# Optimization experiments

Hardware: AMD Instinct MI355X
Metric: run time of the kernel (lower is better)

Reference implementation:

```python
import jax, jax.numpy as jnp
import numpy as np

B = 4096
D_IN = 2048
D_H = 2048
W_SCALE = 0.02  # keep exp() gate pre-activations small / numerically safe


def setup_inputs() -> dict:
    key = jax.random.key(0)
    ks = jax.random.split(key, 16)
    inp = {
        "x": jax.random.normal(ks[0], (B, D_IN), jnp.float32),
        "h_prev": jax.random.normal(ks[1], (B, D_H), jnp.float32),
        "c_prev": jax.random.normal(ks[2], (B, D_H), jnp.float32),
        "n_prev": jax.random.uniform(ks[3], (B, D_H), jnp.float32),
    }
    # input->hidden weights (stored [in, out]; torch Linear computes x @ W.T + b,
    # equivalent to x @ W_here + b) and biases
    for i, name in enumerate(["i", "f", "o", "z"]):
        inp[f"W_{name}"] = jax.random.normal(ks[4 + i], (D_IN, D_H), jnp.float32) * W_SCALE
        inp[f"b_{name}"] = jax.random.normal(ks[8 + i], (D_H,), jnp.float32) * W_SCALE
        inp[f"U_{name}"] = jax.random.normal(ks[12 + i], (D_H, D_H), jnp.float32) * W_SCALE
    return inp


def reference(x, h_prev, c_prev, n_prev,
              W_i, b_i, U_i, W_f, b_f, U_f,
              W_o, b_o, U_o, W_z, b_z, U_z):
    # Gate pre-activations: 8 GEMMs fused pairwise per gate
    i = jnp.exp(x @ W_i + b_i + h_prev @ U_i)
    f = jnp.exp(x @ W_f + b_f + h_prev @ U_f)
    o = jax.nn.sigmoid(x @ W_o + b_o + h_prev @ U_o)
    z = jnp.tanh(x @ W_z + b_z + h_prev @ U_z)
    c = f * c_prev + i * z
    n = f * n_prev + i
    h = o * (c / (n + 1e-6))
    return (h, c, n)
```

## Files before the change

kernel.cpp:

```cpp
#include <hip/hip_runtime.h>
#include <hip/hip_bf16.h>
#include <stdint.h>

#define B_DIM 4096
#define DH    2048
#define K_DIM 4096
#define N_DIM 8192

typedef __bf16  bf16x8 __attribute__((ext_vector_type(8)));
typedef float   f32x4  __attribute__((ext_vector_type(4)));

__device__ __forceinline__ unsigned short f2bf(float f) {
  unsigned int u = __float_as_uint(f);
  u += 0x7FFFu + ((u >> 16) & 1u);
  return (unsigned short)(u >> 16);
}

__global__ void cast_cat_A(const float* __restrict__ x, const float* __restrict__ h,
                           unsigned short* __restrict__ Abuf) {
  int idx = blockIdx.x * 256 + threadIdx.x;
  const int half = B_DIM * (DH / 4);
  bool isx = (idx < half);
  int i2 = isx ? idx : idx - half;
  int b  = i2 >> 9;
  int c4 = i2 & 511;
  const float* src = (isx ? x : h) + (((size_t)b) << 11) + (c4 << 2);
  float4 v = *(const float4*)src;
  ushort4 o;
  o.x = f2bf(v.x); o.y = f2bf(v.y); o.z = f2bf(v.z); o.w = f2bf(v.w);
  int col = (isx ? 0 : DH) + (c4 << 2);
  *(ushort4*)(Abuf + (size_t)b * K_DIM + col) = o;
}

__global__ void transpose_cast_B(const float* __restrict__ Wi, const float* __restrict__ Ui,
                                 const float* __restrict__ Wf, const float* __restrict__ Uf,
                                 const float* __restrict__ Wo, const float* __restrict__ Uo,
                                 const float* __restrict__ Wz, const float* __restrict__ Uz,
                                 unsigned short* __restrict__ Bt) {
  __shared__ unsigned short lds[64 * 68];
  const int k0 = blockIdx.x * 64;
  const int n0 = blockIdx.y * 64;
  const int g  = n0 >> 11;
  const int j0 = n0 & 2047;
  const float* W = (g == 0) ? Wi : (g == 1) ? Wf : (g == 2) ? Wo : Wz;
  const float* U = (g == 0) ? Ui : (g == 1) ? Uf : (g == 2) ? Uo : Uz;
  const float* src = ((k0 < DH) ? (W + (size_t)k0 * DH)
                                : (U + (size_t)(k0 - DH) * DH)) + j0;
  const int t = threadIdx.x;
  #pragma unroll
  for (int r = 0; r < 4; ++r) {
    int slot = r * 256 + t;
    int kk = slot >> 4;
    int c4 = slot & 15;
    float4 v = *(const float4*)(src + (size_t)kk * DH + (c4 << 2));
    int n = c4 << 2;
    lds[(n + 0) * 68 + kk] = f2bf(v.x);
    lds[(n + 1) * 68 + kk] = f2bf(v.y);
    lds[(n + 2) * 68 + kk] = f2bf(v.z);
    lds[(n + 3) * 68 + kk] = f2bf(v.w);
  }
  __syncthreads();
  #pragma unroll
  for (int r = 0; r < 4; ++r) {
    int slot = r * 256 + t;
    int nn = slot >> 4;
    int c8 = slot & 15;
    *(ushort4*)(Bt + (size_t)(n0 + nn) * K_DIM + k0 + (c8 << 2)) =
        *(const ushort4*)(lds + nn * 68 + (c8 << 2));
  }
}

__global__ __launch_bounds__(256, 3) void gemm_bt(const unsigned short* __restrict__ A,
                                                  const unsigned short* __restrict__ Bt,
                                                  float* __restrict__ C) {
  __shared__ alignas(16) unsigned short As[128 * 32];
  __shared__ alignas(16) unsigned short Bs[128 * 32];
  const int t    = threadIdx.x;
  const int wave = t >> 6;
  const int lane = t & 63;
  const int m0 = blockIdx.y * 128;
  const int n0 = blockIdx.x * 128;
  const int wm = (wave & 1) * 64;
  const int wn = (wave >> 1) * 64;
  const int lm = lane & 15;
  const int kg = lane >> 4;

  f32x4 acc[4][4] = {};

  const int c0 = t, c1 = t + 256;
  const unsigned short* pa0 = A  + (size_t)(m0 + (c0 >> 2)) * K_DIM + (c0 & 3) * 8;
  const unsigned short* pa1 = A  + (size_t)(m0 + (c1 >> 2)) * K_DIM + (c1 & 3) * 8;
  const unsigned short* pb0 = Bt + (size_t)(n0 + (c0 >> 2)) * K_DIM + (c0 & 3) * 8;
  const unsigned short* pb1 = Bt + (size_t)(n0 + (c1 >> 2)) * K_DIM + (c1 & 3) * 8;
  unsigned short* lA0 = As + (wave * 64) * 8;
  unsigned short* lA1 = As + (256 + wave * 64) * 8;
  unsigned short* lB0 = Bs + (wave * 64) * 8;
  unsigned short* lB1 = Bs + (256 + wave * 64) * 8;

  const int aoff = (wm + lm) * 32 + kg * 8;
  const int boff = (wn + lm) * 32 + kg * 8;

  for (int k0 = 0; k0 < K_DIM; k0 += 32) {
    __builtin_amdgcn_global_load_lds((const __attribute__((address_space(1))) unsigned int*)(pa0 + k0),
                                     (__attribute__((address_space(3))) unsigned int*)lA0, 16, 0, 0);
    __builtin_amdgcn_global_load_lds((const __attribute__((address_space(1))) unsigned int*)(pa1 + k0),
                                     (__attribute__((address_space(3))) unsigned int*)lA1, 16, 0, 0);
    __builtin_amdgcn_global_load_lds((const __attribute__((address_space(1))) unsigned int*)(pb0 + k0),
                                     (__attribute__((address_space(3))) unsigned int*)lB0, 16, 0, 0);
    __builtin_amdgcn_global_load_lds((const __attribute__((address_space(1))) unsigned int*)(pb1 + k0),
                                     (__attribute__((address_space(3))) unsigned int*)lB1, 16, 0, 0);
    __syncthreads();
    bf16x8 av[4], bv[4];
    #pragma unroll
    for (int mi = 0; mi < 4; ++mi)
      av[mi] = *(const bf16x8*)(As + aoff + mi * 16 * 32);
    #pragma unroll
    for (int ni = 0; ni < 4; ++ni)
      bv[ni] = *(const bf16x8*)(Bs + boff + ni * 16 * 32);
    #pragma unroll
    for (int mi = 0; mi < 4; ++mi) {
      #pragma unroll
      for (int ni = 0; ni < 4; ++ni)
        acc[mi][ni] = __builtin_amdgcn_mfma_f32_16x16x32_bf16(av[mi], bv[ni], acc[mi][ni], 0, 0, 0);
    }
    __syncthreads();
  }

  #pragma unroll
  for (int mi = 0; mi < 4; ++mi) {
    #pragma unroll
    for (int ni = 0; ni < 4; ++ni) {
      float* p = C + (size_t)(m0 + wm + mi * 16 + kg * 4) * N_DIM + (n0 + wn + ni * 16 + lm);
      #pragma unroll
      for (int r = 0; r < 4; ++r)
        p[(size_t)r * N_DIM] = acc[mi][ni][r];
    }
  }
}

__global__ void gate_epilogue(const float* __restrict__ C,
                              const float* __restrict__ bi, const float* __restrict__ bfv,
                              const float* __restrict__ bo, const float* __restrict__ bz,
                              const float* __restrict__ cprev, const float* __restrict__ nprev,
                              float* __restrict__ out) {
  int idx = blockIdx.x * 256 + threadIdx.x;
  int b = idx >> 9;
  int j = (idx & 511) << 2;
  const float* base = C + (size_t)b * N_DIM + j;
  float4 pi = *(const float4*)(base);
  float4 pf = *(const float4*)(base + DH);
  float4 po = *(const float4*)(base + 2 * DH);
  float4 pz = *(const float4*)(base + 3 * DH);
  float4 vbi = *(const float4*)(bi + j);
  float4 vbf = *(const float4*)(bfv + j);
  float4 vbo = *(const float4*)(bo + j);
  float4 vbz = *(const float4*)(bz + j);
  size_t pidx = (((size_t)b) << 11) + j;
  float4 cp = *(const float4*)(cprev + pidx);
  float4 np = *(const float4*)(nprev + pidx);

  const float* Pi = (const float*)&pi; const float* Pf = (const float*)&pf;
  const float* Po = (const float*)&po; const float* Pz = (const float*)&pz;
  const float* Bi = (const float*)&vbi; const float* Bf = (const float*)&vbf;
  const float* Bo = (const float*)&vbo; const float* Bz = (const float*)&vbz;
  const float* Cp = (const float*)&cp; const float* Np = (const float*)&np;

  float rh[4], rc[4], rn[4];
  #pragma unroll
  for (int e = 0; e < 4; ++e) {
    float iv = __expf(Pi[e] + Bi[e]);
    float fv = __expf(Pf[e] + Bf[e]);
    float ao = Po[e] + Bo[e];
    float ov = 1.0f / (1.0f + __expf(-ao));
    float t2 = __expf(2.0f * (Pz[e] + Bz[e]));
    float zv = 1.0f - 2.0f / (t2 + 1.0f);
    float cv = fv * Cp[e] + iv * zv;
    float nv = fv * Np[e] + iv;
    rc[e] = cv; rn[e] = nv;
    rh[e] = ov * (cv / (nv + 1e-6f));
  }
  *(float4*)(out + pidx)            = make_float4(rh[0], rh[1], rh[2], rh[3]);
  *(float4*)(out + 8388608 + pidx)  = make_float4(rc[0], rc[1], rc[2], rc[3]);
  *(float4*)(out + 16777216 + pidx) = make_float4(rn[0], rn[1], rn[2], rn[3]);
}

extern "C" void kernel_launch(void* const* d_in, const int* in_sizes, int n_in,
                              void* d_out, int out_size, void* d_ws, size_t ws_size,
                              hipStream_t stream) {
  const float* x      = (const float*)d_in[0];
  const float* h_prev = (const float*)d_in[1];
  const float* c_prev = (const float*)d_in[2];
  const float* n_prev = (const float*)d_in[3];
  const float* W_i = (const float*)d_in[4];  const float* b_i = (const float*)d_in[5];  const float* U_i = (const float*)d_in[6];
  const float* W_f = (const float*)d_in[7];  const float* b_f = (const float*)d_in[8];  const float* U_f = (const float*)d_in[9];
  const float* W_o = (const float*)d_in[10]; const float* b_o = (const float*)d_in[11]; const float* U_o = (const float*)d_in[12];
  const float* W_z = (const float*)d_in[13]; const float* b_z = (const float*)d_in[14]; const float* U_z = (const float*)d_in[15];
  float* out = (float*)d_out;

  char* ws = (char*)d_ws;
  unsigned short* Abuf = (unsigned short*)ws;
  unsigned short* Bt   = (unsigned short*)(ws + 33554432);
  float*          Cpre = (float*)(ws + 33554432 + 67108864);

  cast_cat_A<<<16384, 256, 0, stream>>>(x, h_prev, Abuf);
  transpose_cast_B<<<dim3(64, 128), 256, 0, stream>>>(W_i, U_i, W_f, U_f, W_o, U_o, W_z, U_z, Bt);
  gemm_bt<<<dim3(64, 32), 256, 0, stream>>>(Abuf, Bt, Cpre);
  gate_epilogue<<<8192, 256, 0, stream>>>(Cpre, b_i, b_f, b_o, b_z, c_prev, n_prev, out);
}
```

Baseline: 649.9 us.

## Interleave gate columns in Bt and fuse gate epilogue into GEMM

Reorders the transposed weight rows so that each wave's four 16-column MFMA tiles hold the i, f, o, z gates for the same hidden units. The gate nonlinearities and state updates can then run directly on the GEMM accumulators. This removes the 128MB fp32 pre-activation buffer write and reread, along with the separate epilogue launch. In exchange, the epilogue now does scalar, strided global loads and stores per lane instead of float4 accesses, and adds register pressure to the GEMM kernel.

```diff
diff --git a/kernel.cpp b/kernel.cpp
--- a/kernel.cpp
+++ b/kernel.cpp
@@ -39,9 +39,8 @@
                                  unsigned short* __restrict__ Bt) {
   __shared__ unsigned short lds[64 * 68];
   const int k0 = blockIdx.x * 64;
-  const int n0 = blockIdx.y * 64;
-  const int g  = n0 >> 11;
-  const int j0 = n0 & 2047;
+  const int g  = blockIdx.y >> 5;
+  const int j0 = (blockIdx.y & 31) * 64;
   const float* W = (g == 0) ? Wi : (g == 1) ? Wf : (g == 2) ? Wo : Wz;
   const float* U = (g == 0) ? Ui : (g == 1) ? Uf : (g == 2) ? Uo : Uz;
   const float* src = ((k0 < DH) ? (W + (size_t)k0 * DH)
@@ -65,14 +64,19 @@
     int slot = r * 256 + t;
     int nn = slot >> 4;
     int c8 = slot & 15;
-    *(ushort4*)(Bt + (size_t)(n0 + nn) * K_DIM + k0 + (c8 << 2)) =
+    int j  = j0 + nn;
+    int np = ((j >> 5) << 7) + ((j & 16) << 2) + (g << 4) + (j & 15);
+    *(ushort4*)(Bt + (size_t)np * K_DIM + k0 + (c8 << 2)) =
         *(const ushort4*)(lds + nn * 68 + (c8 << 2));
   }
 }
 
-__global__ __launch_bounds__(256, 3) void gemm_bt(const unsigned short* __restrict__ A,
-                                                  const unsigned short* __restrict__ Bt,
-                                                  float* __restrict__ C) {
+__global__ __launch_bounds__(256, 3) void gemm_gates(const unsigned short* __restrict__ A,
+                                                     const unsigned short* __restrict__ Bt,
+                                                     const float* __restrict__ bi, const float* __restrict__ bf,
+                                                     const float* __restrict__ bo, const float* __restrict__ bz,
+                                                     const float* __restrict__ cprev, const float* __restrict__ nprev,
+                                                     float* __restrict__ out) {
   __shared__ alignas(16) unsigned short As[128 * 32];
   __shared__ alignas(16) unsigned short Bs[128 * 32];
   const int t    = threadIdx.x;
@@ -126,62 +130,30 @@
     __syncthreads();
   }
 
+  const int jj = (blockIdx.x << 5) + ((wn >> 6) << 4) + lm;
+  const float vbi = bi[jj], vbf = bf[jj], vbo = bo[jj], vbz = bz[jj];
   #pragma unroll
   for (int mi = 0; mi < 4; ++mi) {
+    const int mrow = m0 + wm + mi * 16 + kg * 4;
     #pragma unroll
-    for (int ni = 0; ni < 4; ++ni) {
-      float* p = C + (size_t)(m0 + wm + mi * 16 + kg * 4) * N_DIM + (n0 + wn + ni * 16 + lm);
-      #pragma unroll
-      for (int r = 0; r < 4; ++r)
-        p[(size_t)r * N_DIM] = acc[mi][ni][r];
+    for (int r = 0; r < 4; ++r) {
+      const size_t idx = (size_t)(mrow + r) * DH + jj;
+      float pi = acc[mi][0][r] + vbi;
+      float pf = acc[mi][1][r] + vbf;
+      float po = acc[mi][2][r] + vbo;
+      float pz = acc[mi][3][r] + vbz;
+      float iv = __expf(pi);
+      float fv = __expf(pf);
+      float ov = 1.0f / (1.0f + __expf(-po));
+      float t2 = __expf(2.0f * pz);
+      float zv = 1.0f - 2.0f / (t2 + 1.0f);
+      float cv = fv * cprev[idx] + iv * zv;
+      float nv = fv * nprev[idx] + iv;
+      out[idx]            = ov * (cv / (nv + 1e-6f));
+      out[8388608 + idx]  = cv;
+      out[16777216 + idx] = nv;
     }
   }
-}
-
-__global__ void gate_epilogue(const float* __restrict__ C,
-                              const float* __restrict__ bi, const float* __restrict__ bfv,
-                              const float* __restrict__ bo, const float* __restrict__ bz,
-                              const float* __restrict__ cprev, const float* __restrict__ nprev,
-                              float* __restrict__ out) {
-  int idx = blockIdx.x * 256 + threadIdx.x;
-  int b = idx >> 9;
-  int j = (idx & 511) << 2;
-  const float* base = C + (size_t)b * N_DIM + j;
-  float4 pi = *(const float4*)(base);
-  float4 pf = *(const float4*)(base + DH);
-  float4 po = *(const float4*)(base + 2 * DH);
-  float4 pz = *(const float4*)(base + 3 * DH);
-  float4 vbi = *(const float4*)(bi + j);
-  float4 vbf = *(const float4*)(bfv + j);
-  float4 vbo = *(const float4*)(bo + j);
-  float4 vbz = *(const float4*)(bz + j);
-  size_t pidx = (((size_t)b) << 11) + j;
-  float4 cp = *(const float4*)(cprev + pidx);
-  float4 np = *(const float4*)(nprev + pidx);
-
-  const float* Pi = (const float*)&pi; const float* Pf = (const float*)&pf;
-  const float* Po = (const float*)&po; const float* Pz = (const float*)&pz;
-  const float* Bi = (const float*)&vbi; const float* Bf = (const float*)&vbf;
-  const float* Bo = (const float*)&vbo; const float* Bz = (const float*)&vbz;
-  const float* Cp = (const float*)&cp; const float* Np = (const float*)&np;
-
-  float rh[4], rc[4], rn[4];
-  #pragma unroll
-  for (int e = 0; e < 4; ++e) {
-    float iv = __expf(Pi[e] + Bi[e]);
-    float fv = __expf(Pf[e] + Bf[e]);
-    float ao = Po[e] + Bo[e];
-    float ov = 1.0f / (1.0f + __expf(-ao));
-    float t2 = __expf(2.0f * (Pz[e] + Bz[e]));
-    float zv = 1.0f - 2.0f / (t2 + 1.0f);
-    float cv = fv * Cp[e] + iv * zv;
-    float nv = fv * Np[e] + iv;
-    rc[e] = cv; rn[e] = nv;
-    rh[e] = ov * (cv / (nv + 1e-6f));
-  }
-  *(float4*)(out + pidx)            = make_float4(rh[0], rh[1], rh[2], rh[3]);
-  *(float4*)(out + 8388608 + pidx)  = make_float4(rc[0], rc[1], rc[2], rc[3]);
-  *(float4*)(out + 16777216 + pidx) = make_float4(rn[0], rn[1], rn[2], rn[3]);
 }
 
 extern "C" void kernel_launch(void* const* d_in, const int* in_sizes, int n_in,
@@ -200,10 +172,8 @@
   char* ws = (char*)d_ws;
   unsigned short* Abuf = (unsigned short*)ws;
   unsigned short* Bt   = (unsigned short*)(ws + 33554432);
-  float*          Cpre = (float*)(ws + 33554432 + 67108864);
 
   cast_cat_A<<<16384, 256, 0, stream>>>(x, h_prev, Abuf);
   transpose_cast_B<<<dim3(64, 128), 256, 0, stream>>>(W_i, U_i, W_f, U_f, W_o, U_o, W_z, U_z, Bt);
-  gemm_bt<<<dim3(64, 32), 256, 0, stream>>>(Abuf, Bt, Cpre);
-  gate_epilogue<<<8192, 256, 0, stream>>>(Cpre, b_i, b_f, b_o, b_z, c_prev, n_prev, out);
+  gemm_gates<<<dim3(64, 32), 256, 0, stream>>>(Abuf, Bt, b_i, b_f, b_o, b_z, c_prev, n_prev, out);
 }
```

Measured after the change: 626.3 us. 3.6% less time.
